# Kernel tuning notes

Hardware: AMD Instinct MI355X
Metric: run time of the kernel (lower is better)

## Reference

```python
import jax, jax.numpy as jnp
import numpy as np
from jax import lax

N = 16384       # input points
STRIDE = 4
M = N // STRIDE # sampled centers (single batch: n_o = [o[0]//stride])
NSAMPLE = 16
CIN = 64
COUT = 128
EPS = 1e-5      # BatchNorm1d default eps


def setup_inputs() -> dict:
    key = jax.random.key(0)
    k1, k2, k3, k4 = jax.random.split(key, 4)
    p = jax.random.normal(k1, (N, 3), dtype=jnp.float32)
    n = jax.random.normal(k2, (N, 3), dtype=jnp.float32)
    x = jax.random.normal(k3, (N, CIN), dtype=jnp.float32)
    o = jnp.array([N], dtype=jnp.int32)  # single point cloud
    W = jax.random.normal(k4, (COUT, 3 + CIN), dtype=jnp.float32) * 0.05
    gamma = jnp.ones((COUT,), dtype=jnp.float32)
    beta = jnp.zeros((COUT,), dtype=jnp.float32)
    return {"p": p, "n": n, "x": x, "o": o, "W": W, "gamma": gamma, "beta": beta}


def _fps(p, m):
    """Furthest point sampling (pointops.furthestsampling), single batch."""
    npts = p.shape[0]
    def step(carry, _):
        dists, last = carry
        d = jnp.sum((p - p[last]) ** 2, axis=-1)
        dists = jnp.minimum(dists, d)
        nxt = jnp.argmax(dists).astype(jnp.int32)
        return (dists, nxt), nxt
    first = jnp.int32(0)
    init = (jnp.full((npts,), 1e10, dtype=p.dtype), first)
    _, rest = lax.scan(step, init, None, length=m - 1)
    return jnp.concatenate([first[None], rest])  # [m]


def reference(p, n, x, o, W, gamma, beta):
    # --- furthest sampling: n_o = [o[0]//stride] = [M] (static for single batch)
    idx = _fps(p, M)                      # [M] int32
    n_p = p[idx]                          # [M,3] new coords
    n_n = n[idx]                          # [M,3] new normals
    # --- queryandgroup: kNN of each center in full cloud, use_xyz=True
    d2 = (jnp.sum(n_p * n_p, -1)[:, None]
          + jnp.sum(p * p, -1)[None, :]
          - 2.0 * n_p @ p.T)              # [M,N]
    _, knn = lax.top_k(-lax.stop_gradient(d2), NSAMPLE)   # [M,NSAMPLE]
    grouped_xyz = p[knn] - n_p[:, None, :]                # [M,NS,3] relative coords
    grouped_x = x[knn]                                    # [M,NS,CIN]
    feat = jnp.concatenate([grouped_xyz, grouped_x], axis=-1)  # [M,NS,3+CIN]
    # --- linear (no bias) -> BN (training stats, per channel) -> ReLU -> max over neighbors
    y = jnp.einsum('msc,oc->mso', feat, W)                # [M,NS,COUT]
    mean = jnp.mean(y, axis=(0, 1))
    var = jnp.mean((y - mean) ** 2, axis=(0, 1))          # biased var (torch BN)
    y = (y - mean) * lax.rsqrt(var + EPS) * gamma + beta
    y = jax.nn.relu(y)
    y = jnp.max(y, axis=1)                                # MaxPool1d(nsample) -> [M,COUT]
    n_o = jnp.array([M], dtype=jnp.int32)
    return (n_p, n_n, y, n_o)
```

## Files before the change

### kernel.cpp

```cpp
#include <hip/hip_runtime.h>
#include <math.h>

#define N_PTS 16384
#define M_CTR 4096
#define NS 16
#define CIN 64
#define COUT 128
#define CFEAT 67
#define CPB 4

#define CMB_MAX(va, ia, vb, ib) do { \
    bool _b = ((vb) > (va)) || ((vb) == (va) && (ib) < (ia)); \
    (va) = _b ? (vb) : (va); (ia) = _b ? (ib) : (ia); \
} while (0)

#define DPP_STEP(CTRL) do { \
    int _ovb = __builtin_amdgcn_update_dpp(0xbf800000, __float_as_int(bv), CTRL, 0xF, 0xF, false); \
    int _oib = __builtin_amdgcn_update_dpp(0x7fffffff, bi, CTRL, 0xF, 0xF, false); \
    float _ov = __int_as_float(_ovb); \
    CMB_MAX(bv, bi, _ov, _oib); \
} while (0)

__global__ __launch_bounds__(512, 2) void fps_kernel(const float* __restrict__ p,
                                                     int* __restrict__ sel)
{
    const int tid = threadIdx.x;

    float px[32], py[32], pz[32], dist[32];
#pragma unroll
    for (int k = 0; k < 32; ++k) {
        int j = tid + (k << 9);
        px[k] = p[j*3+0]; py[k] = p[j*3+1]; pz[k] = p[j*3+2];
        dist[k] = 1e10f;
    }

    __shared__ float2 sw[2][8];

    if (tid == 0) sel[0] = 0;
    float qx = p[0], qy = p[1], qz = p[2];

    for (int it = 1; it < M_CTR; ++it) {
        float bv = -1.0f; int bk = 0;
#pragma unroll
        for (int k = 0; k < 32; ++k) {
            float dx = __fsub_rn(px[k], qx);
            float dy = __fsub_rn(py[k], qy);
            float dz = __fsub_rn(pz[k], qz);
            float d2 = __fadd_rn(__fadd_rn(__fmul_rn(dx,dx), __fmul_rn(dy,dy)),
                                 __fmul_rn(dz,dz));
            float nd = fminf(dist[k], d2);
            dist[k] = nd;
            bool b = nd > bv;
            bv = b ? nd : bv;
            bk = b ? k : bk;
        }
        int bi = tid + (bk << 9);

        DPP_STEP(0x111);
        DPP_STEP(0x112);
        DPP_STEP(0x114);
        DPP_STEP(0x118);
        DPP_STEP(0x142);
        DPP_STEP(0x143);

        int par = it & 1;
        if ((tid & 63) == 63) sw[par][tid >> 6] = make_float2(bv, __int_as_float(bi));
        __syncthreads();

        float2 c0 = sw[par][0], c1 = sw[par][1], c2 = sw[par][2], c3 = sw[par][3];
        float2 c4 = sw[par][4], c5 = sw[par][5], c6 = sw[par][6], c7 = sw[par][7];
        float v0 = c0.x, v1 = c1.x, v2 = c2.x, v3 = c3.x;
        float v4 = c4.x, v5 = c5.x, v6 = c6.x, v7 = c7.x;
        int   j0 = __float_as_int(c0.y), j1 = __float_as_int(c1.y);
        int   j2 = __float_as_int(c2.y), j3 = __float_as_int(c3.y);
        int   j4 = __float_as_int(c4.y), j5 = __float_as_int(c5.y);
        int   j6 = __float_as_int(c6.y), j7 = __float_as_int(c7.y);
        CMB_MAX(v0, j0, v1, j1); CMB_MAX(v2, j2, v3, j3);
        CMB_MAX(v4, j4, v5, j5); CMB_MAX(v6, j6, v7, j7);
        CMB_MAX(v0, j0, v2, j2); CMB_MAX(v4, j4, v6, j6);
        CMB_MAX(v0, j0, v4, j4);
        int last = j0;

        if (tid == 0) sel[it] = last;

        int ul = __builtin_amdgcn_readfirstlane(last);
        qx = p[ul*3+0]; qy = p[ul*3+1]; qz = p[ul*3+2];
    }
}

__global__ void prep_kernel(const float* __restrict__ p, const float* __restrict__ nrm,
                            const int* __restrict__ sel, float* __restrict__ pp2,
                            float* __restrict__ out)
{
    int i = blockIdx.x * blockDim.x + threadIdx.x;
    if (i < N_PTS) {
        float x = p[i*3], y = p[i*3+1], z = p[i*3+2];
        pp2[i] = __fadd_rn(__fadd_rn(__fmul_rn(x,x), __fmul_rn(y,y)), __fmul_rn(z,z));
    }
    if (i < M_CTR) {
        int j = sel[i];
        out[i*3+0] = p[j*3+0]; out[i*3+1] = p[j*3+1]; out[i*3+2] = p[j*3+2];
        out[12288 + i*3+0] = nrm[j*3+0];
        out[12288 + i*3+1] = nrm[j*3+1];
        out[12288 + i*3+2] = nrm[j*3+2];
    }
    if (i == 0) out[548864] = (float)M_CTR;
}

__global__ __launch_bounds__(256) void knn_kernel(const float* __restrict__ p,
                                                  const float* __restrict__ pp2,
                                                  const float* __restrict__ np ,
                                                  int* __restrict__ knn)
{
    const int lane = threadIdx.x & 63;
    const int wave = threadIdx.x >> 6;
    const int c = blockIdx.x * 4 + wave;

    float cx = np[c*3], cy = np[c*3+1], cz = np[c*3+2];
    float c2 = __fadd_rn(__fadd_rn(__fmul_rn(cx,cx), __fmul_rn(cy,cy)), __fmul_rn(cz,cz));

    float hd[16]; int hi[16];
#pragma unroll
    for (int k = 0; k < 16; ++k) { hd[k] = 1e30f; hi[k] = 0x7fffffff; }

    for (int t = 0; t < N_PTS/64; ++t) {
        int j = t*64 + lane;
        float px = p[j*3+0], py = p[j*3+1], pz = p[j*3+2];
        float dot = __fadd_rn(__fadd_rn(__fmul_rn(cx,px), __fmul_rn(cy,py)),
                              __fmul_rn(cz,pz));
        float d2  = __fsub_rn(__fadd_rn(c2, pp2[j]), __fmul_rn(2.0f, dot));
        if (d2 < hd[15]) {
#pragma unroll
            for (int k = 15; k >= 1; --k) {
                bool up   = d2 < hd[k-1];
                bool here = d2 < hd[k];
                hd[k] = up ? hd[k-1] : (here ? d2 : hd[k]);
                hi[k] = up ? hi[k-1] : (here ? j  : hi[k]);
            }
            if (d2 < hd[0]) { hd[0] = d2; hi[0] = j; }
        }
    }

    for (int r = 0; r < 16; ++r) {
        float wv = hd[0]; int wi = hi[0];
#pragma unroll
        for (int m = 1; m < 64; m <<= 1) {
            float ov = __shfl_xor(wv, m);
            int   oi = __shfl_xor(wi, m);
            bool b = (ov < wv) || (ov == wv && oi < wi);
            wv = b ? ov : wv; wi = b ? oi : wi;
        }
        if (hi[0] == wi) {
            knn[c*16 + r] = wi;
#pragma unroll
            for (int k = 0; k < 15; ++k) { hd[k] = hd[k+1]; hi[k] = hi[k+1]; }
            hd[15] = 1e30f; hi[15] = 0x7fffffff;
        }
    }
}

__global__ __launch_bounds__(128) void passA_kernel(const float* __restrict__ p,
                                                    const float* __restrict__ xf,
                                                    const float* __restrict__ W,
                                                    const int* __restrict__ knn,
                                                    const float* __restrict__ out ,
                                                    float* __restrict__ ymax,
                                                    float* __restrict__ ymin,
                                                    float* __restrict__ partials)
{
    __shared__ float Wt[CFEAT][COUT];
    __shared__ float ft[CPB][NS][CFEAT];
    __shared__ float bsum[CPB][COUT], bssq[CPB][COUT];

    const int t = threadIdx.x;
    const int mbase = blockIdx.x * CPB;

    for (int c = 0; c < CFEAT; ++c) Wt[c][t] = W[t*CFEAT + c];

    {
        int r = t >> 1, half = t & 1;
        int ci = r >> 4, s = r & 15;
        int m = mbase + ci;
        int nb = knn[m*NS + s];
        if (half == 0) {
            ft[ci][s][0] = __fsub_rn(p[nb*3+0], out[m*3+0]);
            ft[ci][s][1] = __fsub_rn(p[nb*3+1], out[m*3+1]);
            ft[ci][s][2] = __fsub_rn(p[nb*3+2], out[m*3+2]);
        }
        for (int c = half*32; c < half*32 + 32; ++c)
            ft[ci][s][3+c] = xf[nb*CIN + c];
    }
    __syncthreads();

    const int ci = t >> 5, l = t & 31;
    float acc[NS][4];
#pragma unroll
    for (int s = 0; s < NS; ++s) { acc[s][0]=0.f; acc[s][1]=0.f; acc[s][2]=0.f; acc[s][3]=0.f; }

    for (int c = 0; c < CFEAT; ++c) {
        float w0 = Wt[c][l], w1 = Wt[c][l+32], w2 = Wt[c][l+64], w3 = Wt[c][l+96];
#pragma unroll
        for (int s = 0; s < NS; ++s) {
            float f = ft[ci][s][c];
            acc[s][0] = fmaf(f, w0, acc[s][0]);
            acc[s][1] = fmaf(f, w1, acc[s][1]);
            acc[s][2] = fmaf(f, w2, acc[s][2]);
            acc[s][3] = fmaf(f, w3, acc[s][3]);
        }
    }

    const int m = mbase + ci;
#pragma unroll
    for (int j = 0; j < 4; ++j) {
        int o = l + 32*j;
        float s = 0.f, q = 0.f, mx = -1e30f, mn = 1e30f;
#pragma unroll
        for (int sidx = 0; sidx < NS; ++sidx) {
            float v = acc[sidx][j];
            s += v; q = fmaf(v, v, q);
            mx = fmaxf(mx, v); mn = fminf(mn, v);
        }
        bsum[ci][o] = s;
        bssq[ci][o] = q;
        ymax[m*COUT + o] = mx;
        ymin[m*COUT + o] = mn;
    }
    __syncthreads();
    if (t < COUT) {
        float s = bsum[0][t] + bsum[1][t] + bsum[2][t] + bsum[3][t];
        float q = bssq[0][t] + bssq[1][t] + bssq[2][t] + bssq[3][t];
        partials[t*1024          + blockIdx.x] = s;
        partials[(COUT + t)*1024 + blockIdx.x] = q;
    }
}

__global__ __launch_bounds__(256) void bnstat_kernel(const float* __restrict__ partials,
                                                     const float* __restrict__ gamma,
                                                     const float* __restrict__ beta,
                                                     float* __restrict__ scaleshift)
{
    __shared__ float red[256];
    int t = threadIdx.x;
    const float4* v4 = (const float4*)(partials + t*1024);
    float s = 0.f;
    for (int i = 0; i < 256; ++i) {
        float4 v = v4[i];
        s += v.x; s += v.y; s += v.z; s += v.w;
    }
    red[t] = s;
    __syncthreads();
    if (t < COUT) {
        const float inv = 1.0f / 65536.0f;
        float mean = red[t] * inv;
        float var  = red[COUT + t] * inv - mean*mean;
        float rstd = rsqrtf(var + 1e-5f);
        float g = gamma[t] * rstd;
        scaleshift[t]        = g;
        scaleshift[COUT + t] = beta[t] - mean * g;
    }
}

__global__ void final_kernel(float* __restrict__ y ,
                             const float* __restrict__ ymin,
                             const float* __restrict__ scaleshift)
{
    int i = blockIdx.x * blockDim.x + threadIdx.x;
    if (i >= M_CTR * COUT) return;
    int o = i & (COUT - 1);
    float a = scaleshift[o], b = scaleshift[COUT + o];
    float v = (a >= 0.f) ? y[i] : ymin[i];
    float z = fmaf(a, v, b);
    y[i] = fmaxf(z, 0.f);
}

extern "C" void kernel_launch(void* const* d_in, const int* in_sizes, int n_in,
                              void* d_out, int out_size, void* d_ws, size_t ws_size,
                              hipStream_t stream)
{
    const float* p     = (const float*)d_in[0];
    const float* nrm   = (const float*)d_in[1];
    const float* xf    = (const float*)d_in[2];
    const float* W     = (const float*)d_in[4];
    const float* gamma = (const float*)d_in[5];
    const float* beta  = (const float*)d_in[6];

    float* out = (float*)d_out;
    char* ws = (char*)d_ws;
    int*   sel        = (int*)(ws + 0);
    float* pp2        = (float*)(ws + 16384);
    int*   knn        = (int*)(ws + 81920);
    float* ymin       = (float*)(ws + 344064);
    float* partials   = (float*)(ws + 2441216);
    float* scaleshift = (float*)(ws + 3489792);

    float* ymax = out + 24576;

    fps_kernel  <<<1,    512,  0, stream>>>(p, sel);
    prep_kernel <<<64,   256,  0, stream>>>(p, nrm, sel, pp2, out);
    knn_kernel  <<<1024, 256,  0, stream>>>(p, pp2, out, knn);
    passA_kernel<<<M_CTR/CPB, 128, 0, stream>>>(p, xf, W, knn, out, ymax, ymin, partials);
    bnstat_kernel<<<1,   256,  0, stream>>>(partials, gamma, beta, scaleshift);
    final_kernel<<<2048, 256,  0, stream>>>(ymax, ymin, scaleshift);
}
```

Baseline: 7.604 ms.

## Use spatial grid cells with bounding-box pruning in furthest point sampling

Bins points into an 8x8x8 grid, sorts them by cell, and records a per-cell bounding box. Each FPS iteration then updates only cells whose bounding box could lie closer to the new center than that cell's current max distance. Per-cell maxima are kept as packed 64-bit keys updated with atomics, and the argmax is reduced over cells. This targets the single-block FPS loop that updates all 16384 distances every iteration. In exchange it adds several preprocessing kernels, global-memory distance traffic and atomic/worklist overhead, and pruning efficiency depends on the point distribution.

Result: slower. 9.751 ms (+28.2%).

```diff
diff --git a/kernel.cpp b/kernel.cpp
--- a/kernel.cpp
+++ b/kernel.cpp
@@ -8,82 +8,224 @@
 #define COUT 128
 #define CFEAT 67
 #define CPB 4
-
-#define CMB_MAX(va, ia, vb, ib) do { \
-    bool _b = ((vb) > (va)) || ((vb) == (va) && (ib) < (ia)); \
-    (va) = _b ? (vb) : (va); (ia) = _b ? (ib) : (ia); \
-} while (0)
-
-#define DPP_STEP(CTRL) do { \
-    int _ovb = __builtin_amdgcn_update_dpp(0xbf800000, __float_as_int(bv), CTRL, 0xF, 0xF, false); \
-    int _oib = __builtin_amdgcn_update_dpp(0x7fffffff, bi, CTRL, 0xF, 0xF, false); \
-    float _ov = __int_as_float(_ovb); \
-    CMB_MAX(bv, bi, _ov, _oib); \
-} while (0)
-
-__global__ __launch_bounds__(512, 2) void fps_kernel(const float* __restrict__ p,
-                                                     int* __restrict__ sel)
-{
-    const int tid = threadIdx.x;
-
-    float px[32], py[32], pz[32], dist[32];
-#pragma unroll
-    for (int k = 0; k < 32; ++k) {
-        int j = tid + (k << 9);
-        px[k] = p[j*3+0]; py[k] = p[j*3+1]; pz[k] = p[j*3+2];
-        dist[k] = 1e10f;
-    }
-
-    __shared__ float2 sw[2][8];
-
-    if (tid == 0) sel[0] = 0;
+#define NCELL 512
+
+__device__ __forceinline__ unsigned ordu(float f) {
+    unsigned b = __float_as_uint(f);
+    return (b & 0x80000000u) ? ~b : (b | 0x80000000u);
+}
+__device__ __forceinline__ float unord(unsigned u) {
+    unsigned b = (u & 0x80000000u) ? (u & 0x7FFFFFFFu) : ~u;
+    return __uint_as_float(b);
+}
+__device__ __forceinline__ unsigned long long ullmax2(unsigned long long a, unsigned long long b) {
+    return b > a ? b : a;
+}
+
+__global__ void init_kernel(float* __restrict__ dist, unsigned* __restrict__ bmin,
+                            unsigned* __restrict__ bmax, int* __restrict__ cnt,
+                            int* __restrict__ fill)
+{
+    int i = blockIdx.x * blockDim.x + threadIdx.x;
+    if (i < N_PTS) dist[i] = 1e10f;
+    if (i < NCELL * 3) { bmin[i] = 0xFFFFFFFFu; bmax[i] = 0u; }
+    if (i < NCELL) { cnt[i] = 0; fill[i] = 0; }
+}
+
+__global__ __launch_bounds__(256) void bbox_kernel(const float* __restrict__ p,
+                                                   float* __restrict__ gbb)
+{
+    int t = threadIdx.x, lane = t & 63, w = t >> 6;
+    float mnx = 1e30f, mny = 1e30f, mnz = 1e30f;
+    float mxx = -1e30f, mxy = -1e30f, mxz = -1e30f;
+    for (int i = t; i < N_PTS; i += 256) {
+        float x = p[i*3], y = p[i*3+1], z = p[i*3+2];
+        mnx = fminf(mnx, x); mny = fminf(mny, y); mnz = fminf(mnz, z);
+        mxx = fmaxf(mxx, x); mxy = fmaxf(mxy, y); mxz = fmaxf(mxz, z);
+    }
+    for (int m = 1; m < 64; m <<= 1) {
+        mnx = fminf(mnx, __shfl_xor(mnx, m)); mny = fminf(mny, __shfl_xor(mny, m));
+        mnz = fminf(mnz, __shfl_xor(mnz, m));
+        mxx = fmaxf(mxx, __shfl_xor(mxx, m)); mxy = fmaxf(mxy, __shfl_xor(mxy, m));
+        mxz = fmaxf(mxz, __shfl_xor(mxz, m));
+    }
+    __shared__ float s[4][6];
+    if (lane == 0) { s[w][0]=mnx; s[w][1]=mny; s[w][2]=mnz; s[w][3]=mxx; s[w][4]=mxy; s[w][5]=mxz; }
+    __syncthreads();
+    if (t == 0) {
+        float a0 = fminf(fminf(s[0][0], s[1][0]), fminf(s[2][0], s[3][0]));
+        float a1 = fminf(fminf(s[0][1], s[1][1]), fminf(s[2][1], s[3][1]));
+        float a2 = fminf(fminf(s[0][2], s[1][2]), fminf(s[2][2], s[3][2]));
+        float a3 = fmaxf(fmaxf(s[0][3], s[1][3]), fmaxf(s[2][3], s[3][3]));
+        float a4 = fmaxf(fmaxf(s[0][4], s[1][4]), fmaxf(s[2][4], s[3][4]));
+        float a5 = fmaxf(fmaxf(s[0][5], s[1][5]), fmaxf(s[2][5], s[3][5]));
+        gbb[0]=a0; gbb[1]=a1; gbb[2]=a2; gbb[3]=a3; gbb[4]=a4; gbb[5]=a5;
+    }
+}
+
+__global__ void assign_kernel(const float* __restrict__ p, const float* __restrict__ gbb,
+                              int* __restrict__ c_of, int* __restrict__ cnt)
+{
+    int i = blockIdx.x * blockDim.x + threadIdx.x;
+    if (i >= N_PTS) return;
+    float bx = gbb[0], by = gbb[1], bz = gbb[2];
+    float sx = 7.9999f / fmaxf(gbb[3] - bx, 1e-20f);
+    float sy = 7.9999f / fmaxf(gbb[4] - by, 1e-20f);
+    float sz = 7.9999f / fmaxf(gbb[5] - bz, 1e-20f);
+    float x = p[i*3], y = p[i*3+1], z = p[i*3+2];
+    int ix = min(7, max(0, (int)((x - bx) * sx)));
+    int iy = min(7, max(0, (int)((y - by) * sy)));
+    int iz = min(7, max(0, (int)((z - bz) * sz)));
+    int c = (ix << 6) | (iy << 3) | iz;
+    c_of[i] = c;
+    atomicAdd(&cnt[c], 1);
+}
+
+__global__ __launch_bounds__(512) void prefix_kernel(const int* __restrict__ cnt,
+                                                     int* __restrict__ start)
+{
+    __shared__ int a[NCELL];
+    int t = threadIdx.x;
+    int v = cnt[t]; a[t] = v; __syncthreads();
+    for (int off = 1; off < NCELL; off <<= 1) {
+        int u = (t >= off) ? a[t - off] : 0;
+        __syncthreads();
+        a[t] += u;
+        __syncthreads();
+    }
+    start[t] = a[t] - v;
+}
+
+__global__ void scatter_kernel(const float* __restrict__ p, const int* __restrict__ c_of,
+                               const int* __restrict__ start, int* __restrict__ fill,
+                               float4* __restrict__ sp, unsigned* __restrict__ bmin,
+                               unsigned* __restrict__ bmax)
+{
+    int i = blockIdx.x * blockDim.x + threadIdx.x;
+    if (i >= N_PTS) return;
+    int c = c_of[i];
+    int pos = start[c] + atomicAdd(&fill[c], 1);
+    float x = p[i*3], y = p[i*3+1], z = p[i*3+2];
+    sp[pos] = make_float4(x, y, z, __int_as_float(i));
+    atomicMin(&bmin[c*3+0], ordu(x)); atomicMax(&bmax[c*3+0], ordu(x));
+    atomicMin(&bmin[c*3+1], ordu(y)); atomicMax(&bmax[c*3+1], ordu(y));
+    atomicMin(&bmin[c*3+2], ordu(z)); atomicMax(&bmax[c*3+2], ordu(z));
+}
+
+__global__ __launch_bounds__(512) void fps_kernel(const float* __restrict__ p,
+                                                  const float4* __restrict__ sp,
+                                                  float* __restrict__ dist,
+                                                  const int* __restrict__ g_cstart,
+                                                  const int* __restrict__ g_ccnt,
+                                                  const unsigned* __restrict__ g_bmin,
+                                                  const unsigned* __restrict__ g_bmax,
+                                                  int* __restrict__ sel)
+{
+    __shared__ float4 bbmn[NCELL], bbmx[NCELL];
+    __shared__ unsigned long long key[NCELL];
+    __shared__ int cst[NCELL], ccn[NCELL];
+    __shared__ int wl[832];
+    __shared__ int wlc;
+    __shared__ unsigned long long skw[8];
+
+    const int t = threadIdx.x;
+    const int lane = t & 63, wave = t >> 6;
+
+    {
+        cst[t] = g_cstart[t]; ccn[t] = g_ccnt[t];
+        bbmn[t] = make_float4(unord(g_bmin[t*3]), unord(g_bmin[t*3+1]), unord(g_bmin[t*3+2]), 0.f);
+        bbmx[t] = make_float4(unord(g_bmax[t*3]), unord(g_bmax[t*3+1]), unord(g_bmax[t*3+2]), 0.f);
+        key[t] = 0ull;
+    }
+    if (t == 0) { wlc = 0; sel[0] = 0; }
     float qx = p[0], qy = p[1], qz = p[2];
+    __syncthreads();
 
     for (int it = 1; it < M_CTR; ++it) {
-        float bv = -1.0f; int bk = 0;
-#pragma unroll
-        for (int k = 0; k < 32; ++k) {
-            float dx = __fsub_rn(px[k], qx);
-            float dy = __fsub_rn(py[k], qy);
-            float dz = __fsub_rn(pz[k], qz);
-            float d2 = __fadd_rn(__fadd_rn(__fmul_rn(dx,dx), __fmul_rn(dy,dy)),
-                                 __fmul_rn(dz,dz));
-            float nd = fminf(dist[k], d2);
-            dist[k] = nd;
-            bool b = nd > bv;
-            bv = b ? nd : bv;
-            bk = b ? k : bk;
-        }
-        int bi = tid + (bk << 9);
-
-        DPP_STEP(0x111);
-        DPP_STEP(0x112);
-        DPP_STEP(0x114);
-        DPP_STEP(0x118);
-        DPP_STEP(0x142);
-        DPP_STEP(0x143);
-
-        int par = it & 1;
-        if ((tid & 63) == 63) sw[par][tid >> 6] = make_float2(bv, __int_as_float(bi));
+        {
+            int cnt = ccn[t];
+            bool active = false;
+            if (cnt > 0) {
+                float4 mn = bbmn[t], mx = bbmx[t];
+                float ddx = fmaxf(fmaxf(__fsub_rn(mn.x, qx), __fsub_rn(qx, mx.x)), 0.f);
+                float ddy = fmaxf(fmaxf(__fsub_rn(mn.y, qy), __fsub_rn(qy, mx.y)), 0.f);
+                float ddz = fmaxf(fmaxf(__fsub_rn(mn.z, qz), __fsub_rn(qz, mx.z)), 0.f);
+                float dmin = __fadd_rn(__fadd_rn(__fmul_rn(ddx,ddx), __fmul_rn(ddy,ddy)),
+                                       __fmul_rn(ddz,ddz));
+                float cm = __uint_as_float((unsigned)(key[t] >> 32));
+                active = (it == 1) || (dmin < cm * 1.00001f);
+            }
+            if (active) {
+                key[t] = 0ull;
+                int st = cst[t];
+                int nch = (cnt + 63) >> 6;
+                int base = atomicAdd(&wlc, nch);
+                for (int b = 0; b < nch; ++b) wl[base + b] = (t << 14) | (st + (b << 6));
+            }
+        }
         __syncthreads();
-
-        float2 c0 = sw[par][0], c1 = sw[par][1], c2 = sw[par][2], c3 = sw[par][3];
-        float2 c4 = sw[par][4], c5 = sw[par][5], c6 = sw[par][6], c7 = sw[par][7];
-        float v0 = c0.x, v1 = c1.x, v2 = c2.x, v3 = c3.x;
-        float v4 = c4.x, v5 = c5.x, v6 = c6.x, v7 = c7.x;
-        int   j0 = __float_as_int(c0.y), j1 = __float_as_int(c1.y);
-        int   j2 = __float_as_int(c2.y), j3 = __float_as_int(c3.y);
-        int   j4 = __float_as_int(c4.y), j5 = __float_as_int(c5.y);
-        int   j6 = __float_as_int(c6.y), j7 = __float_as_int(c7.y);
-        CMB_MAX(v0, j0, v1, j1); CMB_MAX(v2, j2, v3, j3);
-        CMB_MAX(v4, j4, v5, j5); CMB_MAX(v6, j6, v7, j7);
-        CMB_MAX(v0, j0, v2, j2); CMB_MAX(v4, j4, v6, j6);
-        CMB_MAX(v0, j0, v4, j4);
-        int last = j0;
-
-        if (tid == 0) sel[it] = last;
-
-        int ul = __builtin_amdgcn_readfirstlane(last);
+        int nwl = wlc;
+
+        for (int e0 = wave; e0 < nwl; e0 += 16) {
+            int m0 = wl[e0]; int c0 = m0 >> 14, s0 = m0 & 16383;
+            int len0 = min(64, cst[c0] + ccn[c0] - s0);
+            bool a0 = lane < len0;
+            float4 P0; float D0;
+            if (a0) { P0 = sp[s0 + lane]; D0 = dist[s0 + lane]; }
+
+            int e1 = e0 + 8; bool h1 = e1 < nwl;
+            int c1 = 0, s1 = 0, len1 = 0; bool a1 = false;
+            float4 P1; float D1;
+            if (h1) {
+                int m1 = wl[e1]; c1 = m1 >> 14; s1 = m1 & 16383;
+                len1 = min(64, cst[c1] + ccn[c1] - s1);
+                a1 = lane < len1;
+                if (a1) { P1 = sp[s1 + lane]; D1 = dist[s1 + lane]; }
+            }
+
+            unsigned long long k0 = 0ull;
+            if (a0) {
+                float dx = __fsub_rn(P0.x, qx), dy = __fsub_rn(P0.y, qy), dz = __fsub_rn(P0.z, qz);
+                float d2 = __fadd_rn(__fadd_rn(__fmul_rn(dx,dx), __fmul_rn(dy,dy)),
+                                     __fmul_rn(dz,dz));
+                float nd = fminf(D0, d2);
+                dist[s0 + lane] = nd;
+                k0 = ((unsigned long long)__float_as_uint(nd) << 32)
+                   | (unsigned long long)(~(unsigned)__float_as_int(P0.w));
+            }
+            for (int m = 1; m < 64; m <<= 1) k0 = ullmax2(k0, __shfl_xor(k0, m));
+            if (lane == 0) atomicMax(&key[c0], k0);
+
+            if (h1) {
+                unsigned long long k1 = 0ull;
+                if (a1) {
+                    float dx = __fsub_rn(P1.x, qx), dy = __fsub_rn(P1.y, qy), dz = __fsub_rn(P1.z, qz);
+                    float d2 = __fadd_rn(__fadd_rn(__fmul_rn(dx,dx), __fmul_rn(dy,dy)),
+                                         __fmul_rn(dz,dz));
+                    float nd = fminf(D1, d2);
+                    dist[s1 + lane] = nd;
+                    k1 = ((unsigned long long)__float_as_uint(nd) << 32)
+                       | (unsigned long long)(~(unsigned)__float_as_int(P1.w));
+                }
+                for (int m = 1; m < 64; m <<= 1) k1 = ullmax2(k1, __shfl_xor(k1, m));
+                if (lane == 0) atomicMax(&key[c1], k1);
+            }
+        }
+        __syncthreads();
+
+        unsigned long long k = key[t];
+        for (int m = 1; m < 64; m <<= 1) k = ullmax2(k, __shfl_xor(k, m));
+        if (lane == 0) skw[wave] = k;
+        if (t == 0) wlc = 0;
+        __syncthreads();
+        unsigned long long b0 = skw[0], b1 = skw[1], b2 = skw[2], b3 = skw[3];
+        unsigned long long b4 = skw[4], b5 = skw[5], b6 = skw[6], b7 = skw[7];
+        b0 = ullmax2(b0, b1); b2 = ullmax2(b2, b3); b4 = ullmax2(b4, b5); b6 = ullmax2(b6, b7);
+        b0 = ullmax2(b0, b2); b4 = ullmax2(b4, b6);
+        b0 = ullmax2(b0, b4);
+        int widx = (int)(~(unsigned)(b0 & 0xFFFFFFFFull));
+        if (t == 0) sel[it] = widx;
+        int ul = __builtin_amdgcn_readfirstlane(widx);
         qx = p[ul*3+0]; qy = p[ul*3+1]; qz = p[ul*3+2];
     }
 }
@@ -260,7 +402,7 @@
     }
 }
 
-__global__ void final_kernel(float* __restrict__ y ,
+__global__ void final_kernel(float* __restrict__ y,
                              const float* __restrict__ ymin,
                              const float* __restrict__ scaleshift)
 {
@@ -293,12 +435,28 @@
     float* partials   = (float*)(ws + 2441216);
     float* scaleshift = (float*)(ws + 3489792);
 
+    float4*   sp        = (float4*)(ws + 81920);
+    char*     yb        = ws + 344064;
+    float*    dist      = (float*)(yb + 0);
+    int*      c_of      = (int*)(yb + 65536);
+    int*      cellcnt   = (int*)(yb + 131072);
+    int*      cellfill  = (int*)(yb + 133120);
+    int*      cellstart = (int*)(yb + 135168);
+    unsigned* bbmin_u   = (unsigned*)(yb + 137216);
+    unsigned* bbmax_u   = (unsigned*)(yb + 143360);
+    float*    gbb       = (float*)(yb + 149504);
+
     float* ymax = out + 24576;
 
-    fps_kernel  <<<1,    512,  0, stream>>>(p, sel);
-    prep_kernel <<<64,   256,  0, stream>>>(p, nrm, sel, pp2, out);
-    knn_kernel  <<<1024, 256,  0, stream>>>(p, pp2, out, knn);
-    passA_kernel<<<M_CTR/CPB, 128, 0, stream>>>(p, xf, W, knn, out, ymax, ymin, partials);
-    bnstat_kernel<<<1,   256,  0, stream>>>(partials, gamma, beta, scaleshift);
-    final_kernel<<<2048, 256,  0, stream>>>(ymax, ymin, scaleshift);
-}
+    init_kernel   <<<64, 256, 0, stream>>>(dist, bbmin_u, bbmax_u, cellcnt, cellfill);
+    bbox_kernel   <<<1,  256, 0, stream>>>(p, gbb);
+    assign_kernel <<<64, 256, 0, stream>>>(p, gbb, c_of, cellcnt);
+    prefix_kernel <<<1,  512, 0, stream>>>(cellcnt, cellstart);
+    scatter_kernel<<<64, 256, 0, stream>>>(p, c_of, cellstart, cellfill, sp, bbmin_u, bbmax_u);
+    fps_kernel    <<<1,  512, 0, stream>>>(p, sp, dist, cellstart, cellcnt, bbmin_u, bbmax_u, sel);
+    prep_kernel   <<<64, 256, 0, stream>>>(p, nrm, sel, pp2, out);
+    knn_kernel    <<<1024, 256, 0, stream>>>(p, pp2, out, knn);
+    passA_kernel  <<<M_CTR/CPB, 128, 0, stream>>>(p, xf, W, knn, out, ymax, ymin, partials);
+    bnstat_kernel <<<1, 256, 0, stream>>>(partials, gamma, beta, scaleshift);
+    final_kernel  <<<2048, 256, 0, stream>>>(ymax, ymin, scaleshift);
+}
```
